# Optimization experiments

Hardware: AMD Instinct MI355X
Metric: run time of the kernel (lower is better)

The kernel has to match this reference:

```python
import jax, jax.numpy as jnp
import numpy as np

L, D, H, KV, HD, FF, V = 2, 2048, 16, 8, 128, 6144, 32000
B, T = 1, 2048
THETA = 1.0e6
EPS = 1e-6
NEG = -1e30


def _rope_tables():
    inv = 1.0 / (THETA ** (np.arange(0, HD, 2, dtype=np.float32) / HD))
    ang = np.arange(T, dtype=np.float32)[:, None] * inv[None, :]
    ang = np.concatenate([ang, ang], axis=1)  # [T, HD]
    return jnp.asarray(np.cos(ang), jnp.float32), jnp.asarray(np.sin(ang), jnp.float32)


def _rmsnorm(x, scale):
    v = jnp.mean(x * x, axis=-1, keepdims=True)
    return x * jax.lax.rsqrt(v + EPS) * scale


def _rope(x, cos, sin):
    # x: [B, h, T, HD]; rotate-half RoPE with full-dim cos/sin tables
    x1, x2 = x[..., : HD // 2], x[..., HD // 2 :]
    rot = jnp.concatenate([-x2, x1], axis=-1)
    return x * cos[None, None] + rot * sin[None, None]


def setup_inputs() -> dict:
    key = jax.random.key(0)
    ks = jax.random.split(key, 12)
    s = 0.02
    return {
        "token_ids": jax.random.randint(ks[0], (B, T), 0, V),
        "emb": jax.random.normal(ks[1], (V, D), jnp.float32) * s,
        "Wq": jax.random.normal(ks[2], (L, D, H * HD), jnp.float32) * s,
        "Wk": jax.random.normal(ks[3], (L, D, KV * HD), jnp.float32) * s,
        "Wv": jax.random.normal(ks[4], (L, D, KV * HD), jnp.float32) * s,
        "Wo": jax.random.normal(ks[5], (L, H * HD, D), jnp.float32) * s,
        "qn": jnp.ones((L, HD), jnp.float32),
        "kn": jnp.ones((L, HD), jnp.float32),
        "W1": jax.random.normal(ks[6], (L, D, FF), jnp.float32) * s,
        "W2": jax.random.normal(ks[7], (L, D, FF), jnp.float32) * s,
        "W3": jax.random.normal(ks[8], (L, FF, D), jnp.float32) * s,
        "ln1": jnp.ones((L, D), jnp.float32),
        "ln2": jnp.ones((L, D), jnp.float32),
        "lnf": jnp.ones((D,), jnp.float32),
    }


def reference(token_ids, emb, Wq, Wk, Wv, Wo, qn, kn, W1, W2, W3, ln1, ln2, lnf):
    cos, sin = _rope_tables()
    x = emb[token_ids]  # [B, T, D]
    causal = jnp.tril(jnp.ones((T, T), dtype=bool))
    G = H // KV
    scale = 1.0 / np.sqrt(HD)
    for l in range(L):
        # attention block
        h = _rmsnorm(x, ln1[l])
        q = (h @ Wq[l]).reshape(B, T, H, HD).transpose(0, 2, 1, 3)   # [B,H,T,HD]
        k = (h @ Wk[l]).reshape(B, T, KV, HD).transpose(0, 2, 1, 3)  # [B,KV,T,HD]
        v = (h @ Wv[l]).reshape(B, T, KV, HD).transpose(0, 2, 1, 3)
        q = _rmsnorm(q, qn[l])
        k = _rmsnorm(k, kn[l])
        q = _rope(q, cos, sin)
        k = _rope(k, cos, sin)
        qg = q.reshape(B, KV, G, T, HD)
        s_att = jnp.einsum("bgqtd,bgsd->bgqts", qg, k) * scale
        s_att = jnp.where(causal, s_att, NEG)
        a = jax.nn.softmax(s_att, axis=-1)
        o = jnp.einsum("bgqts,bgsd->bgqtd", a, v)
        o = o.reshape(B, H, T, HD).transpose(0, 2, 1, 3).reshape(B, T, H * HD)
        x = x + o @ Wo[l]
        # SwiGLU FFN block
        h = _rmsnorm(x, ln2[l])
        x = x + (jax.nn.silu(h @ W1[l]) * (h @ W2[l])) @ W3[l]
    x = _rmsnorm(x, lnf)
    return x @ emb.T  # tied lm head -> [B, T, V]
```

## Files before the change

kernel.cpp:

```cpp
#include <hip/hip_runtime.h>
#include <math.h>

typedef float f32x4 __attribute__((ext_vector_type(4)));
typedef __bf16 bf16x8 __attribute__((ext_vector_type(8)));
typedef unsigned short u16x8 __attribute__((ext_vector_type(8)));

static constexpr int Dm  = 2048;
static constexpr int Tm  = 2048;
static constexpr int Hm  = 16;
static constexpr int KVm = 8;
static constexpr int HDm = 128;
static constexpr int FFm = 6144;
static constexpr int Vm  = 32000;
static constexpr int QKVN = 4096;

__device__ __forceinline__ float b2f(unsigned short u) {
  unsigned int x = ((unsigned int)u) << 16;
  return __builtin_bit_cast(float, x);
}
__device__ __forceinline__ unsigned short f2b(float f) {
  return __builtin_bit_cast(unsigned short, (__bf16)f);
}
__device__ __forceinline__ f32x4 mfma16x16x32(bf16x8 a, bf16x8 b, f32x4 c) {
  return __builtin_amdgcn_mfma_f32_16x16x32_bf16(a, b, c, 0, 0, 0);
}

__device__ __forceinline__ void gload16(const void* g, void* lds) {
  __builtin_amdgcn_global_load_lds(
      (const __attribute__((address_space(1))) unsigned int*)g,
      (__attribute__((address_space(3))) unsigned int*)lds, 16, 0, 0);
}

__device__ __forceinline__ int xcd_swz(int o, int nwg) {
  int q = nwg >> 3, r8 = nwg & 7;
  int xcd = o & 7, pos = o >> 3;
  return (xcd < r8) ? xcd * (q + 1) + pos : r8 * (q + 1) + (xcd - r8) * q + pos;
}

__global__ void rope_tables_k(float* __restrict__ cosT, float* __restrict__ sinT) {
  int t = blockIdx.x;
  int i = threadIdx.x;
  double inv = pow(1000000.0, -(double)i / 64.0);
  double ang = (double)t * inv;
  cosT[t * 64 + i] = (float)cos(ang);
  sinT[t * 64 + i] = (float)sin(ang);
}

__global__ __launch_bounds__(256) void embed_k(const int* __restrict__ ids,
                                               const float* __restrict__ emb,
                                               float* __restrict__ x) {
  int t = blockIdx.x;
  int d0 = threadIdx.x * 8;
  int id = ids[t];
  const float* src = emb + (size_t)id * Dm + d0;
  float* dst = x + (size_t)t * Dm + d0;
  *(f32x4*)dst       = *(const f32x4*)src;
  *(f32x4*)(dst + 4) = *(const f32x4*)(src + 4);
}

__global__ __launch_bounds__(256) void cvt_flat_k(const float* __restrict__ src,
                                                  unsigned short* __restrict__ dst) {
  size_t i = ((size_t)blockIdx.x * 256 + threadIdx.x) * 8;
  f32x4 a = *(const f32x4*)(src + i);
  f32x4 b = *(const f32x4*)(src + i + 4);
  u16x8 o;
  o[0] = f2b(a.x); o[1] = f2b(a.y); o[2] = f2b(a.z); o[3] = f2b(a.w);
  o[4] = f2b(b.x); o[5] = f2b(b.y); o[6] = f2b(b.z); o[7] = f2b(b.w);
  *(u16x8*)(dst + i) = o;
}

__global__ __launch_bounds__(256) void rmsnorm_k(const float* __restrict__ x,
                                                 const float* __restrict__ g,
                                                 unsigned short* __restrict__ y) {
  int t = blockIdx.x;
  const float* xr = x + (size_t)t * Dm;
  float vals[8];
  float s = 0.f;
#pragma unroll
  for (int i = 0; i < 8; ++i) {
    float vv = xr[threadIdx.x + i * 256];
    vals[i] = vv;
    s += vv * vv;
  }
#pragma unroll
  for (int off = 32; off; off >>= 1) s += __shfl_xor(s, off);
  __shared__ float red[4];
  if ((threadIdx.x & 63) == 0) red[threadIdx.x >> 6] = s;
  __syncthreads();
  s = (red[0] + red[1]) + (red[2] + red[3]);
  float r = rsqrtf(s * (1.f / Dm) + 1e-6f);
  unsigned short* yr = y + (size_t)t * Dm;
#pragma unroll
  for (int i = 0; i < 8; ++i) {
    int d = threadIdx.x + i * 256;
    yr[d] = f2b(vals[i] * r * g[d]);
  }
}

__global__ __launch_bounds__(256) void qknorm_rope_k(unsigned short* __restrict__ q,
                                                     const float* __restrict__ nrm,
                                                     const float* __restrict__ cosT,
                                                     const float* __restrict__ sinT,
                                                     int nheads) {
  int gw = (int)((blockIdx.x * blockDim.x + threadIdx.x) >> 6);
  int lane = threadIdx.x & 63;
  int t = gw / nheads, h = gw % nheads;
  unsigned short* row = q + ((size_t)t * nheads + h) * HDm;
  float x1 = b2f(row[lane]);
  float x2 = b2f(row[lane + 64]);
  float s = x1 * x1 + x2 * x2;
#pragma unroll
  for (int off = 32; off; off >>= 1) s += __shfl_xor(s, off);
  float r = rsqrtf(s * (1.f / HDm) + 1e-6f);
  float y1 = x1 * r * nrm[lane];
  float y2 = x2 * r * nrm[lane + 64];
  float c = cosT[t * 64 + lane];
  float sn = sinT[t * 64 + lane];
  row[lane]      = f2b(y1 * c - y2 * sn);
  row[lane + 64] = f2b(y2 * c + y1 * sn);
}

__global__ __launch_bounds__(256) void cvtT_k(const float* __restrict__ W,
                                              unsigned short* __restrict__ Wt,
                                              int K, int N) {
  __shared__ __align__(16) unsigned short tile[64][68];
  const int n0 = blockIdx.x * 64, k0 = blockIdx.y * 64;
  const int tid = threadIdx.x;
#pragma unroll
  for (int i = 0; i < 4; ++i) {
    int e = tid + i * 256;
    int r = e >> 4, c4 = (e & 15) * 4;
    f32x4 v = *(const f32x4*)(W + (size_t)(k0 + r) * N + n0 + c4);
    tile[r][c4 + 0] = f2b(v.x);
    tile[r][c4 + 1] = f2b(v.y);
    tile[r][c4 + 2] = f2b(v.z);
    tile[r][c4 + 3] = f2b(v.w);
  }
  __syncthreads();
#pragma unroll
  for (int i = 0; i < 2; ++i) {
    int e = tid + i * 256;
    int rr = e >> 3, cc = (e & 7) * 8;
    u16x8 o;
#pragma unroll
    for (int j = 0; j < 8; ++j) o[j] = tile[cc + j][rr];
    *(u16x8*)(Wt + (size_t)(n0 + rr) * K + k0 + cc) = o;
  }
}

template <int EPI, bool BF32, bool OUTF32>
__global__ __launch_bounds__(256) void gemm_k(const unsigned short* __restrict__ A,
                                              const void* __restrict__ B,
                                              void* __restrict__ C,
                                              void* __restrict__ C2,
                                              void* __restrict__ C3,
                                              int N, int K, int cOff) {
  __shared__ __align__(16) unsigned short As[128 * 32];
  __shared__ __align__(16) unsigned short Bs[128 * 32];
  const int tid = threadIdx.x;
  const int nwg = gridDim.x * gridDim.y;
  const int nid = xcd_swz(blockIdx.x + gridDim.x * blockIdx.y, nwg);
  const int bm = nid % gridDim.x, bn = nid / gridDim.x;
  const int w = tid >> 6, lane = tid & 63;
  const int wm = (w >> 1) * 64, wn = (w & 1) * 64;
  const int lr = lane & 15, hi = lane >> 4, kq = hi * 8;
  const int rowA0 = bm * 128, colB0 = bn * 128;

  const int sr = lane >> 2;
  const int sc = (lane & 3) * 8;
  const unsigned short* a0 = A + (size_t)(rowA0 + (w * 2 + 0) * 16 + sr) * K + sc;
  const unsigned short* a1 = A + (size_t)(rowA0 + (w * 2 + 1) * 16 + sr) * K + sc;
  unsigned short* la0 = &As[(w * 2 + 0) * 512];
  unsigned short* la1 = &As[(w * 2 + 1) * 512];
  const unsigned short* b0 = nullptr; const unsigned short* b1 = nullptr;
  unsigned short* lb0 = &Bs[(w * 2 + 0) * 512];
  unsigned short* lb1 = &Bs[(w * 2 + 1) * 512];
  if (!BF32) {
    b0 = (const unsigned short*)B + (size_t)(colB0 + (w * 2 + 0) * 16 + sr) * K + sc;
    b1 = (const unsigned short*)B + (size_t)(colB0 + (w * 2 + 1) * 16 + sr) * K + sc;
  }

  f32x4 acc[4][4] = {};

  for (int k0 = 0; k0 < K; k0 += 32) {
    __syncthreads();
    gload16(a0 + k0, la0);
    gload16(a1 + k0, la1);
    if (!BF32) {
      gload16(b0 + k0, lb0);
      gload16(b1 + k0, lb1);
    } else {
#pragma unroll
      for (int i = 0; i < 2; ++i) {
        int e = tid + i * 256;
        int rr = e >> 2, cc = (e & 3) * 8;
        const float* bp = (const float*)B + (size_t)(colB0 + rr) * K + k0 + cc;
        f32x4 v0 = *(const f32x4*)bp;
        f32x4 v1 = *(const f32x4*)(bp + 4);
        u16x8 o;
        o[0] = f2b(v0.x); o[1] = f2b(v0.y); o[2] = f2b(v0.z); o[3] = f2b(v0.w);
        o[4] = f2b(v1.x); o[5] = f2b(v1.y); o[6] = f2b(v1.z); o[7] = f2b(v1.w);
        *(u16x8*)&Bs[rr * 32 + cc] = o;
      }
    }
    __syncthreads();

    bf16x8 av[4], bv[4];
#pragma unroll
    for (int m = 0; m < 4; ++m)
      av[m] = __builtin_bit_cast(bf16x8, *(const u16x8*)&As[(wm + m * 16 + lr) * 32 + kq]);
#pragma unroll
    for (int n = 0; n < 4; ++n)
      bv[n] = __builtin_bit_cast(bf16x8, *(const u16x8*)&Bs[(wn + n * 16 + lr) * 32 + kq]);
#pragma unroll
    for (int m = 0; m < 4; ++m)
#pragma unroll
      for (int n = 0; n < 4; ++n)
        acc[m][n] = mfma16x16x32(av[m], bv[n], acc[m][n]);
  }

  const int r0 = rowA0 + wm + hi * 4;
  const int c0 = wn + lr;
#pragma unroll
  for (int m = 0; m < 4; ++m)
#pragma unroll
    for (int n = 0; n < 4; ++n) {
      const int cc = colB0 + c0 + n * 16;
#pragma unroll
      for (int j = 0; j < 4; ++j) {
        int r = r0 + m * 16 + j;
        if (EPI == 0) {
          size_t idx = (size_t)r * N + cOff + cc;
          if (OUTF32) ((float*)C)[idx] = acc[m][n][j];
          else        ((unsigned short*)C)[idx] = f2b(acc[m][n][j]);
        } else if (EPI == 1) {
          ((float*)C)[(size_t)r * N + cc] += acc[m][n][j];
        } else if (EPI == 2) {
          unsigned short* Cb = (unsigned short*)C;
          size_t idx = (size_t)r * N + cc;
          float gg = b2f(Cb[idx]);
          gg = gg / (1.f + __expf(-gg));
          Cb[idx] = f2b(gg * acc[m][n][j]);
        } else {
          unsigned short v = f2b(acc[m][n][j]);
          if (cc < 2048)      ((unsigned short*)C )[(size_t)r * 2048 + cc] = v;
          else if (cc < 3072) ((unsigned short*)C2)[(size_t)r * 1024 + (cc - 2048)] = v;
          else                ((unsigned short*)C3)[(size_t)r * 1024 + (cc - 3072)] = v;
        }
      }
    }
}

#define LDA256(MH)                                                             \
  _Pragma("unroll") for (int m_ = 0; m_ < 4; ++m_)                             \
  _Pragma("unroll") for (int ks_ = 0; ks_ < 2; ++ks_)                          \
    av[m_][ks_] = *(const bf16x8*)&Ac[aBase + (MH) * 4096 + m_ * 1024 + uu[ks_]];
#define LDB256(NH)                                                             \
  _Pragma("unroll") for (int n_ = 0; n_ < 2; ++n_)                             \
  _Pragma("unroll") for (int ks_ = 0; ks_ < 2; ++ks_)                          \
    bv[n_][ks_] = *(const bf16x8*)&Bc[bBase + (NH) * 2048 + n_ * 1024 + uu[ks_]];
#define MMA256(MH, NH)                                                         \
  __builtin_amdgcn_s_setprio(1);                                               \
  _Pragma("unroll") for (int m_ = 0; m_ < 4; ++m_)                             \
  _Pragma("unroll") for (int n_ = 0; n_ < 2; ++n_)                             \
  _Pragma("unroll") for (int ks_ = 0; ks_ < 2; ++ks_)                          \
    acc[(MH) * 4 + m_][(NH) * 2 + n_] = mfma16x16x32(                          \
        av[m_][ks_], bv[n_][ks_], acc[(MH) * 4 + m_][(NH) * 2 + n_]);          \
  __builtin_amdgcn_s_setprio(0);
#define SYNCV                                                                  \
  asm volatile("s_waitcnt vmcnt(4)" ::: "memory");                             \
  __builtin_amdgcn_s_barrier();                                                \
  asm volatile("s_waitcnt lgkmcnt(0)" ::: "memory");                           \
  __builtin_amdgcn_sched_barrier(0);
#define SYNCNV                                                                 \
  __builtin_amdgcn_s_barrier();                                                \
  asm volatile("s_waitcnt lgkmcnt(0)" ::: "memory");                           \
  __builtin_amdgcn_sched_barrier(0);
#define ENDPH __builtin_amdgcn_s_barrier();

template <int EPI, bool OUTF32>
__global__ __launch_bounds__(512) void gemm256_k(const unsigned short* __restrict__ A,
                                                 const unsigned short* __restrict__ B,
                                                 void* __restrict__ C,
                                                 int N, int K, int cOff) {
  __shared__ __align__(16) unsigned short lds[2][2][256 * 64];
  const int tid = threadIdx.x;
  const int nwg = gridDim.x * gridDim.y;
  const int nid = xcd_swz(blockIdx.x + gridDim.x * blockIdx.y, nwg);
  const int bm = nid % gridDim.x, bn = nid / gridDim.x;
  const int w = tid >> 6, lane = tid & 63;
  const int wr = w >> 2, wc = w & 3;
  const int lr = lane & 15, hi = lane >> 4;
  const int rowA0 = bm * 256, colB0 = bn * 256;
  const int nk = K >> 6;

  const int srow = lane >> 3;
  const int ulog = (lane & 7) ^ srow;
  const int eaR = (w < 4) ? w * 16 : 128 + (w - 4) * 16;
  const int laR = eaR + 64;
  const int ebR = (w >> 1) * 64 + (w & 1) * 16;
  const int lbR = ebR + 32;
  const unsigned short* gAt = A + (size_t)rowA0 * K + ulog * 8;
  const unsigned short* gBt = B + (size_t)colB0 * K + ulog * 8;

  int uu[2];
  uu[0] = ((0 + hi) ^ (lr & 7)) * 8;
  uu[1] = ((4 + hi) ^ (lr & 7)) * 8;
  const int aBase = (wr * 128 + lr) * 64;
  const int bBase = (wc * 64 + lr) * 64;

  f32x4 acc[8][4] = {};
  bf16x8 av[4][2], bv[2][2];

  auto stage2 = [&](const unsigned short* g, int rbase, unsigned short* l, int k0) {
    gload16(g + (size_t)(rbase + srow) * K + k0, l + rbase * 64);
    gload16(g + (size_t)(rbase + 8 + srow) * K + k0, l + (rbase + 8) * 64);
  };

  stage2(gAt, eaR, &lds[0][0][0], 0);
  stage2(gBt, ebR, &lds[0][1][0], 0);
  stage2(gBt, lbR, &lds[0][1][0], 0);
  stage2(gAt, laR, &lds[0][0][0], 0);
  asm volatile("s_waitcnt vmcnt(0)" ::: "memory");
  __builtin_amdgcn_s_barrier();

  for (int kt = 0; kt < nk; ++kt) {
    unsigned short* Ac = &lds[kt & 1][0][0];
    unsigned short* Bc = &lds[kt & 1][1][0];
    unsigned short* An = &lds[(kt + 1) & 1][0][0];
    unsigned short* Bn = &lds[(kt + 1) & 1][1][0];
    const int k0n = (kt + 1) << 6;
    const bool more = (kt + 1) < nk;

    LDA256(0) LDB256(0)
    if (more) stage2(gAt, eaR, An, k0n);
    SYNCV MMA256(0, 0) ENDPH
    LDB256(1)
    if (more) stage2(gBt, ebR, Bn, k0n);
    SYNCV MMA256(0, 1) ENDPH
    LDA256(1)
    if (more) stage2(gBt, lbR, Bn, k0n);
    SYNCNV MMA256(1, 1) ENDPH
    LDB256(0)
    if (more) stage2(gAt, laR, An, k0n);
    SYNCV MMA256(1, 0) ENDPH
  }

  const int r0 = rowA0 + wr * 128 + hi * 4;
  const int c0 = colB0 + wc * 64 + lr;
#pragma unroll
  for (int mi = 0; mi < 8; ++mi)
#pragma unroll
    for (int n = 0; n < 4; ++n) {
      const int cc = c0 + n * 16;
#pragma unroll
      for (int j = 0; j < 4; ++j) {
        int r = r0 + mi * 16 + j;
        if (EPI == 0) {
          size_t idx = (size_t)r * N + cOff + cc;
          if (OUTF32) ((float*)C)[idx] = acc[mi][n][j];
          else        ((unsigned short*)C)[idx] = f2b(acc[mi][n][j]);
        } else {
          unsigned short* Cb = (unsigned short*)C;
          size_t idx = (size_t)r * N + cc;
          float gg = b2f(Cb[idx]);
          gg = gg / (1.f + __expf(-gg));
          Cb[idx] = f2b(gg * acc[mi][n][j]);
        }
      }
    }
}

__global__ __launch_bounds__(256) void attn_k(const unsigned short* __restrict__ qg,
                                              const unsigned short* __restrict__ kg,
                                              const unsigned short* __restrict__ vg,
                                              unsigned short* __restrict__ og) {
  __shared__ __align__(16) unsigned short Ks[64 * 128];
  __shared__ __align__(16) unsigned short Vt[128 * 72];
  __shared__ __align__(16) unsigned short Pl[4 * 16 * 72];
  const int tid = threadIdx.x;
  const int nid = xcd_swz(blockIdx.x + (blockIdx.y << 4), 256);
  const int pr = nid & 15, h = nid >> 4;
  const int w = tid >> 6, lane = tid & 63;
  const int lr = lane & 15, hi = lane >> 4;
  const int kvh = h >> 1;

  size_t goff[4]; unsigned kdst[4]; int vr[4], vc[4];
#pragma unroll
  for (int i = 0; i < 4; ++i) {
    int e = tid + i * 256;
    int r = e >> 4, c = (e & 15) * 8;
    goff[i] = ((size_t)r * KVm + kvh) * HDm + c;
    kdst[i] = (unsigned)((r * 256 + c * 2) ^ ((r & 7) << 4));
    vr[i] = r; vc[i] = c;
  }

  for (int pass = 0; pass < 2; ++pass) {
    const int qt = pass ? (31 - pr) : pr;
    const int t0 = qt * 64;
    const int ntk = qt + 1;

    bf16x8 qa[4];
    {
      const unsigned short* qrow = qg + ((size_t)(t0 + w * 16 + lr) * Hm + h) * HDm;
#pragma unroll
      for (int ks = 0; ks < 4; ++ks)
        qa[ks] = __builtin_bit_cast(bf16x8, *(const u16x8*)(qrow + ks * 32 + hi * 8));
    }

    f32x4 oa[8] = {};
    float mj[4], lj[4];
#pragma unroll
    for (int j = 0; j < 4; ++j) { mj[j] = -3.0e38f; lj[j] = 0.f; }

    u16x8 kk[4], vv[4];
#pragma unroll
    for (int i = 0; i < 4; ++i) {
      kk[i] = *(const u16x8*)(kg + goff[i]);
      vv[i] = *(const u16x8*)(vg + goff[i]);
    }

    for (int t = 0; t < ntk; ++t) {
      __syncthreads();
#pragma unroll
      for (int i = 0; i < 4; ++i) {
        *(u16x8*)((char*)Ks + kdst[i]) = kk[i];
#pragma unroll
        for (int j = 0; j < 8; ++j) {
          int d = vc[i] + j;
          Vt[d * 72 + (vr[i] ^ (((d >> 3) & 7) << 3))] = vv[i][j];
        }
      }
      if (t + 1 < ntk) {
        size_t add = (size_t)(t + 1) * 64 * KVm * HDm;
#pragma unroll
        for (int i = 0; i < 4; ++i) {
          kk[i] = *(const u16x8*)(kg + goff[i] + add);
          vv[i] = *(const u16x8*)(vg + goff[i] + add);
        }
      }
      __syncthreads();

      const int s0 = t * 64;
      f32x4 s[4] = {};
#pragma unroll
      for (int ks = 0; ks < 4; ++ks)
#pragma unroll
        for (int nt = 0; nt < 4; ++nt) {
          int krow = nt * 16 + lr;
          int kbyte = (krow * 256 + (ks * 32 + hi * 8) * 2) ^ ((krow & 7) << 4);
          bf16x8 kf = __builtin_bit_cast(bf16x8, *(const u16x8*)((char*)Ks + kbyte));
          s[nt] = mfma16x16x32(qa[ks], kf, s[nt]);
        }

      float p[4][4];
      const bool maskt = (t == ntk - 1);
#pragma unroll
      for (int nt = 0; nt < 4; ++nt)
#pragma unroll
        for (int j = 0; j < 4; ++j) {
          float val = s[nt][j] * 0.08838834764831845f;
          if (maskt && (s0 + nt * 16 + lr) > (t0 + w * 16 + hi * 4 + j)) val = -1e30f;
          p[nt][j] = val;
        }

#pragma unroll
      for (int j = 0; j < 4; ++j) {
        float mx = fmaxf(fmaxf(p[0][j], p[1][j]), fmaxf(p[2][j], p[3][j]));
#pragma unroll
        for (int msk = 1; msk < 16; msk <<= 1) mx = fmaxf(mx, __shfl_xor(mx, msk));
        float mnew = fmaxf(mj[j], mx);
        float alpha = __expf(mj[j] - mnew);
        mj[j] = mnew;
        float sum = 0.f;
#pragma unroll
        for (int nt = 0; nt < 4; ++nt) {
          float e = __expf(p[nt][j] - mnew);
          p[nt][j] = e;
          sum += e;
        }
#pragma unroll
        for (int msk = 1; msk < 16; msk <<= 1) sum += __shfl_xor(sum, msk);
        lj[j] = lj[j] * alpha + sum;
#pragma unroll
        for (int nt2 = 0; nt2 < 8; ++nt2) oa[nt2][j] *= alpha;
      }

#pragma unroll
      for (int nt = 0; nt < 4; ++nt)
#pragma unroll
        for (int j = 0; j < 4; ++j)
          Pl[(w * 16 + hi * 4 + j) * 72 + nt * 16 + lr] = f2b(p[nt][j]);
      __builtin_amdgcn_sched_barrier(0);

      bf16x8 pa[2];
#pragma unroll
      for (int ks2 = 0; ks2 < 2; ++ks2)
        pa[ks2] = __builtin_bit_cast(bf16x8,
                   *(const u16x8*)&Pl[(w * 16 + lr) * 72 + ks2 * 32 + hi * 8]);
#pragma unroll
      for (int nt2 = 0; nt2 < 8; ++nt2)
#pragma unroll
        for (int ks2 = 0; ks2 < 2; ++ks2) {
          int d = nt2 * 16 + lr;
          int kv = ks2 * 32 + hi * 8;
          bf16x8 vf = __builtin_bit_cast(bf16x8,
                       *(const u16x8*)&Vt[d * 72 + (kv ^ (((d >> 3) & 7) << 3))]);
          oa[nt2] = mfma16x16x32(pa[ks2], vf, oa[nt2]);
        }
    }

#pragma unroll
    for (int nt2 = 0; nt2 < 8; ++nt2)
#pragma unroll
      for (int j = 0; j < 4; ++j) {
        int row = t0 + w * 16 + hi * 4 + j;
        int d = nt2 * 16 + lr;
        og[((size_t)row * Hm + h) * HDm + d] = f2b(oa[nt2][j] / lj[j]);
      }
  }
}

extern "C" void kernel_launch(void* const* d_in, const int* in_sizes, int n_in,
                              void* d_out, int out_size, void* d_ws, size_t ws_size,
                              hipStream_t stream) {
  (void)in_sizes; (void)n_in; (void)out_size; (void)ws_size;
  const int*   ids = (const int*)d_in[0];
  const float* emb = (const float*)d_in[1];
  const float* Wq  = (const float*)d_in[2];
  const float* Wk  = (const float*)d_in[3];
  const float* Wv  = (const float*)d_in[4];
  const float* Wo  = (const float*)d_in[5];
  const float* qn  = (const float*)d_in[6];
  const float* kn  = (const float*)d_in[7];
  const float* W1  = (const float*)d_in[8];
  const float* W2  = (const float*)d_in[9];
  const float* W3  = (const float*)d_in[10];
  const float* ln1 = (const float*)d_in[11];
  const float* ln2 = (const float*)d_in[12];
  const float* lnf = (const float*)d_in[13];

  char* p = (char*)d_ws;
  float* xf          = (float*)p;          p += (size_t)Tm * Dm * 4;
  unsigned short* hb = (unsigned short*)p; p += (size_t)Tm * Dm * 2;
  float* cosT        = (float*)p;          p += (size_t)Tm * 64 * 4;
  float* sinT        = (float*)p;          p += (size_t)Tm * 64 * 4;
  unsigned short* qb = (unsigned short*)p; p += (size_t)Tm * Hm * HDm * 2;
  unsigned short* kb = (unsigned short*)p; p += (size_t)Tm * KVm * HDm * 2;
  unsigned short* vb = (unsigned short*)p; p += (size_t)Tm * KVm * HDm * 2;
  unsigned short* ob = (unsigned short*)p; p += (size_t)Tm * Hm * HDm * 2;
  unsigned short* wt = (unsigned short*)p; p += (size_t)Dm * FFm * 2;
  unsigned short* g1 = qb;

  rope_tables_k<<<Tm, 64, 0, stream>>>(cosT, sinT);
  embed_k<<<Tm, 256, 0, stream>>>(ids, emb, xf);

  for (int l = 0; l < 2; ++l) {
    const float* Wq_l = Wq + (size_t)l * Dm * (Hm * HDm);
    const float* Wk_l = Wk + (size_t)l * Dm * (KVm * HDm);
    const float* Wv_l = Wv + (size_t)l * Dm * (KVm * HDm);
    const float* Wo_l = Wo + (size_t)l * (Hm * HDm) * Dm;
    const float* W1_l = W1 + (size_t)l * Dm * FFm;
    const float* W2_l = W2 + (size_t)l * Dm * FFm;
    const float* W3_l = W3 + (size_t)l * FFm * Dm;

    rmsnorm_k<<<Tm, 256, 0, stream>>>(xf, ln1 + (size_t)l * Dm, hb);

    cvtT_k<<<dim3((Hm * HDm) / 64, Dm / 64), 256, 0, stream>>>(Wq_l, wt, Dm, Hm * HDm);
    cvtT_k<<<dim3((KVm * HDm) / 64, Dm / 64), 256, 0, stream>>>(
        Wk_l, wt + (size_t)2048 * Dm, Dm, KVm * HDm);
    cvtT_k<<<dim3((KVm * HDm) / 64, Dm / 64), 256, 0, stream>>>(
        Wv_l, wt + (size_t)3072 * Dm, Dm, KVm * HDm);
    gemm_k<3, false, false><<<dim3(Tm / 128, QKVN / 128), 256, 0, stream>>>(
        hb, wt, qb, kb, vb, QKVN, Dm, 0);

    qknorm_rope_k<<<(Tm * Hm) / 4, 256, 0, stream>>>(qb, qn + (size_t)l * HDm, cosT, sinT, Hm);
    qknorm_rope_k<<<(Tm * KVm) / 4, 256, 0, stream>>>(kb, kn + (size_t)l * HDm, cosT, sinT, KVm);

    attn_k<<<dim3(16, 16), 256, 0, stream>>>(qb, kb, vb, ob);

    cvtT_k<<<dim3(Dm / 64, (Hm * HDm) / 64), 256, 0, stream>>>(Wo_l, wt, Hm * HDm, Dm);
    gemm_k<1, false, false><<<dim3(Tm / 128, Dm / 128), 256, 0, stream>>>(
        ob, wt, xf, nullptr, nullptr, Dm, Hm * HDm, 0);

    rmsnorm_k<<<Tm, 256, 0, stream>>>(xf, ln2 + (size_t)l * Dm, hb);

    cvtT_k<<<dim3(FFm / 64, Dm / 64), 256, 0, stream>>>(W1_l, wt, Dm, FFm);
    gemm256_k<0, false><<<dim3(Tm / 256, FFm / 256), 512, 0, stream>>>(
        hb, wt, g1, FFm, Dm, 0);
    cvtT_k<<<dim3(FFm / 64, Dm / 64), 256, 0, stream>>>(W2_l, wt, Dm, FFm);
    gemm256_k<2, false><<<dim3(Tm / 256, FFm / 256), 512, 0, stream>>>(
        hb, wt, g1, FFm, Dm, 0);
    cvtT_k<<<dim3(Dm / 64, FFm / 64), 256, 0, stream>>>(W3_l, wt, FFm, Dm);
    gemm_k<1, false, false><<<dim3(Tm / 128, Dm / 128), 256, 0, stream>>>(
        g1, wt, xf, nullptr, nullptr, Dm, FFm, 0);
  }

  rmsnorm_k<<<Tm, 256, 0, stream>>>(xf, lnf, hb);

  unsigned short* embB = qb;
  const int chunks[3] = {12288, 12288, 7424};
  int off = 0;
  for (int c = 0; c < 3; ++c) {
    const int rows = chunks[c];
    cvt_flat_k<<<rows, 256, 0, stream>>>(emb + (size_t)off * Dm, embB);
    gemm256_k<0, true><<<dim3(Tm / 256, rows / 256), 512, 0, stream>>>(
        hb, embB, d_out, Vm, Dm, off);
    off += rows;
  }
}
```

Baseline: 1.553 ms.

## Double-buffer 128x128 GEMM with 64-wide K tiles and swizzled LDS

```diff
diff --git a/kernel.cpp b/kernel.cpp
--- a/kernel.cpp
+++ b/kernel.cpp
@@ -148,75 +148,83 @@
   }
 }
 
-template <int EPI, bool BF32, bool OUTF32>
-__global__ __launch_bounds__(256) void gemm_k(const unsigned short* __restrict__ A,
-                                              const void* __restrict__ B,
-                                              void* __restrict__ C,
-                                              void* __restrict__ C2,
-                                              void* __restrict__ C3,
-                                              int N, int K, int cOff) {
-  __shared__ __align__(16) unsigned short As[128 * 32];
-  __shared__ __align__(16) unsigned short Bs[128 * 32];
+template <int EPI, bool OUTF32>
+__global__ __launch_bounds__(256) void gemm2p_k(const unsigned short* __restrict__ A,
+                                                const unsigned short* __restrict__ B,
+                                                void* __restrict__ C,
+                                                void* __restrict__ C2,
+                                                void* __restrict__ C3,
+                                                int N, int K, int cOff) {
+  __shared__ __align__(16) unsigned short lds[2][2][128 * 64];
   const int tid = threadIdx.x;
   const int nwg = gridDim.x * gridDim.y;
   const int nid = xcd_swz(blockIdx.x + gridDim.x * blockIdx.y, nwg);
   const int bm = nid % gridDim.x, bn = nid / gridDim.x;
   const int w = tid >> 6, lane = tid & 63;
   const int wm = (w >> 1) * 64, wn = (w & 1) * 64;
-  const int lr = lane & 15, hi = lane >> 4, kq = hi * 8;
+  const int lr = lane & 15, hi = lane >> 4;
   const int rowA0 = bm * 128, colB0 = bn * 128;
-
-  const int sr = lane >> 2;
-  const int sc = (lane & 3) * 8;
-  const unsigned short* a0 = A + (size_t)(rowA0 + (w * 2 + 0) * 16 + sr) * K + sc;
-  const unsigned short* a1 = A + (size_t)(rowA0 + (w * 2 + 1) * 16 + sr) * K + sc;
-  unsigned short* la0 = &As[(w * 2 + 0) * 512];
-  unsigned short* la1 = &As[(w * 2 + 1) * 512];
-  const unsigned short* b0 = nullptr; const unsigned short* b1 = nullptr;
-  unsigned short* lb0 = &Bs[(w * 2 + 0) * 512];
-  unsigned short* lb1 = &Bs[(w * 2 + 1) * 512];
-  if (!BF32) {
-    b0 = (const unsigned short*)B + (size_t)(colB0 + (w * 2 + 0) * 16 + sr) * K + sc;
-    b1 = (const unsigned short*)B + (size_t)(colB0 + (w * 2 + 1) * 16 + sr) * K + sc;
-  }
+  const int nk = K >> 6;
+
+  const int srow = lane >> 3;
+  const int ulog = (lane & 7) ^ srow;
+  const unsigned short* gA = A + (size_t)(rowA0 + w * 32 + srow) * K + ulog * 8;
+  const unsigned short* gB = B + (size_t)(colB0 + w * 32 + srow) * K + ulog * 8;
+
+  int uu[2];
+  uu[0] = ((0 + hi) ^ (lr & 7)) * 8;
+  uu[1] = ((4 + hi) ^ (lr & 7)) * 8;
 
   f32x4 acc[4][4] = {};
 
-  for (int k0 = 0; k0 < K; k0 += 32) {
-    __syncthreads();
-    gload16(a0 + k0, la0);
-    gload16(a1 + k0, la1);
-    if (!BF32) {
-      gload16(b0 + k0, lb0);
-      gload16(b1 + k0, lb1);
-    } else {
-#pragma unroll
-      for (int i = 0; i < 2; ++i) {
-        int e = tid + i * 256;
-        int rr = e >> 2, cc = (e & 3) * 8;
-        const float* bp = (const float*)B + (size_t)(colB0 + rr) * K + k0 + cc;
-        f32x4 v0 = *(const f32x4*)bp;
-        f32x4 v1 = *(const f32x4*)(bp + 4);
-        u16x8 o;
-        o[0] = f2b(v0.x); o[1] = f2b(v0.y); o[2] = f2b(v0.z); o[3] = f2b(v0.w);
-        o[4] = f2b(v1.x); o[5] = f2b(v1.y); o[6] = f2b(v1.z); o[7] = f2b(v1.w);
-        *(u16x8*)&Bs[rr * 32 + cc] = o;
-      }
-    }
-    __syncthreads();
-
-    bf16x8 av[4], bv[4];
+  auto stage8 = [&](int buf, int k0) {
+    unsigned short* lA = &lds[buf][0][(w * 32) * 64];
+    unsigned short* lB = &lds[buf][1][(w * 32) * 64];
+#pragma unroll
+    for (int i = 0; i < 4; ++i) {
+      gload16(gA + (size_t)(i * 8) * K + k0, lA + i * 8 * 64);
+      gload16(gB + (size_t)(i * 8) * K + k0, lB + i * 8 * 64);
+    }
+  };
+
+  stage8(0, 0);
+  asm volatile("s_waitcnt vmcnt(0)" ::: "memory");
+  __builtin_amdgcn_s_barrier();
+
+  for (int kt = 0; kt < nk; ++kt) {
+    const int cur = kt & 1;
+    if (kt + 1 < nk) stage8(cur ^ 1, (kt + 1) << 6);
+
+    const unsigned short* Ac = &lds[cur][0][0];
+    const unsigned short* Bc = &lds[cur][1][0];
+    bf16x8 av[4][2], bv[4][2];
+#pragma unroll
+    for (int m = 0; m < 4; ++m) {
+      int rb = (wm + m * 16 + lr) * 64;
+#pragma unroll
+      for (int ks = 0; ks < 2; ++ks)
+        av[m][ks] = *(const bf16x8*)&Ac[rb + uu[ks]];
+    }
+#pragma unroll
+    for (int n = 0; n < 4; ++n) {
+      int rb = (wn + n * 16 + lr) * 64;
+#pragma unroll
+      for (int ks = 0; ks < 2; ++ks)
+        bv[n][ks] = *(const bf16x8*)&Bc[rb + uu[ks]];
+    }
+    __builtin_amdgcn_s_setprio(1);
 #pragma unroll
     for (int m = 0; m < 4; ++m)
-      av[m] = __builtin_bit_cast(bf16x8, *(const u16x8*)&As[(wm + m * 16 + lr) * 32 + kq]);
-#pragma unroll
-    for (int n = 0; n < 4; ++n)
-      bv[n] = __builtin_bit_cast(bf16x8, *(const u16x8*)&Bs[(wn + n * 16 + lr) * 32 + kq]);
-#pragma unroll
-    for (int m = 0; m < 4; ++m)
 #pragma unroll
       for (int n = 0; n < 4; ++n)
-        acc[m][n] = mfma16x16x32(av[m], bv[n], acc[m][n]);
+#pragma unroll
+        for (int ks = 0; ks < 2; ++ks)
+          acc[m][n] = mfma16x16x32(av[m][ks], bv[n][ks], acc[m][n]);
+    __builtin_amdgcn_s_setprio(0);
+
+    asm volatile("s_waitcnt vmcnt(0) lgkmcnt(0)" ::: "memory");
+    __builtin_amdgcn_sched_barrier(0);
+    __builtin_amdgcn_s_barrier();
   }
 
   const int r0 = rowA0 + wm + hi * 4;
@@ -571,7 +579,7 @@
         Wk_l, wt + (size_t)2048 * Dm, Dm, KVm * HDm);
     cvtT_k<<<dim3((KVm * HDm) / 64, Dm / 64), 256, 0, stream>>>(
         Wv_l, wt + (size_t)3072 * Dm, Dm, KVm * HDm);
-    gemm_k<3, false, false><<<dim3(Tm / 128, QKVN / 128), 256, 0, stream>>>(
+    gemm2p_k<3, false><<<dim3(Tm / 128, QKVN / 128), 256, 0, stream>>>(
         hb, wt, qb, kb, vb, QKVN, Dm, 0);
 
     qknorm_rope_k<<<(Tm * Hm) / 4, 256, 0, stream>>>(qb, qn + (size_t)l * HDm, cosT, sinT, Hm);
@@ -580,7 +588,7 @@
     attn_k<<<dim3(16, 16), 256, 0, stream>>>(qb, kb, vb, ob);
 
     cvtT_k<<<dim3(Dm / 64, (Hm * HDm) / 64), 256, 0, stream>>>(Wo_l, wt, Hm * HDm, Dm);
-    gemm_k<1, false, false><<<dim3(Tm / 128, Dm / 128), 256, 0, stream>>>(
+    gemm2p_k<1, false><<<dim3(Tm / 128, Dm / 128), 256, 0, stream>>>(
         ob, wt, xf, nullptr, nullptr, Dm, Hm * HDm, 0);
 
     rmsnorm_k<<<Tm, 256, 0, stream>>>(xf, ln2 + (size_t)l * Dm, hb);
@@ -592,7 +600,7 @@
     gemm256_k<2, false><<<dim3(Tm / 256, FFm / 256), 512, 0, stream>>>(
         hb, wt, g1, FFm, Dm, 0);
     cvtT_k<<<dim3(Dm / 64, FFm / 64), 256, 0, stream>>>(W3_l, wt, FFm, Dm);
-    gemm_k<1, false, false><<<dim3(Tm / 128, Dm / 128), 256, 0, stream>>>(
+    gemm2p_k<1, false><<<dim3(Tm / 128, Dm / 128), 256, 0, stream>>>(
         g1, wt, xf, nullptr, nullptr, Dm, FFm, 0);
   }
 
```

New measurement: 1.430 ms. 1.09x faster.
